# Optimization experiments

Hardware: AMD Instinct MI355X
Metric: run time of the kernel (lower is better)

The kernel has to match this reference:

```python
import jax, jax.numpy as jnp
import numpy as np

B, C, H, W = 2, 192, 96, 96
HEADS, DG, KH, KW = 12, 12, 3, 3
K = KH * KW
PAD, DIL = KH // 2, 1
MLP_HIDDEN = 2 * C  # mlp_ratio = 2


def setup_inputs() -> dict:
    key = jax.random.key(0)
    ks = jax.random.split(key, 14)
    s = 0.02
    return {
        "q": jax.random.normal(ks[0], (B, C, H, W), jnp.float32),
        "k": jax.random.normal(ks[1], (B, C, H, W), jnp.float32),
        "v": jax.random.normal(ks[2], (B, C, H, W), jnp.float32),
        "offset": jax.random.normal(ks[3], (B, DG * 2 * K, H, W), jnp.float32),
        "Wq": jax.random.normal(ks[4], (C, C), jnp.float32) * s,
        "bq": jax.random.normal(ks[5], (C,), jnp.float32) * s,
        "Wk": jax.random.normal(ks[6], (C, C), jnp.float32) * s,
        "bk": jax.random.normal(ks[7], (C,), jnp.float32) * s,
        "Wv": jax.random.normal(ks[8], (C, C), jnp.float32) * s,
        "bv": jax.random.normal(ks[9], (C,), jnp.float32) * s,
        "W1": jax.random.normal(ks[10], (C, MLP_HIDDEN), jnp.float32) * s,
        "b1": jax.random.normal(ks[11], (MLP_HIDDEN,), jnp.float32) * s,
        "W2": jax.random.normal(ks[12], (MLP_HIDDEN, C), jnp.float32) * s,
        "b2": jax.random.normal(ks[13], (C,), jnp.float32) * s,
    }


def _bilinear_sample(img, py, px):
    """img: [B,G,Cg,H,W]; py,px: [B,G,K,H,W] fractional sample coords.
    Returns [B,G,Cg,K,H,W]; zero outside image (DCN-style per-corner masking)."""
    b, g, cg, h, w = img.shape
    y0 = jnp.floor(py)
    x0 = jnp.floor(px)
    wy1 = py - y0
    wx1 = px - x0
    wy0 = 1.0 - wy1
    wx0 = 1.0 - wx1
    imgf = img.reshape(b, g, cg, h * w)

    def corner(yi, xi, wgt):
        valid = ((yi >= 0) & (yi <= h - 1) & (xi >= 0) & (xi <= w - 1)).astype(img.dtype)
        yc = jnp.clip(yi, 0, h - 1).astype(jnp.int32)
        xc = jnp.clip(xi, 0, w - 1).astype(jnp.int32)
        idx = (yc * w + xc).reshape(b, g, 1, -1)  # [B,G,1,K*H*W]
        gth = jnp.take_along_axis(imgf, idx, axis=3)  # [B,G,Cg,K*H*W]
        return gth * (valid * wgt).reshape(b, g, 1, -1)

    out = (corner(y0, x0, wy0 * wx0)
           + corner(y0, x0 + 1, wy0 * wx1)
           + corner(y0 + 1, x0, wy1 * wx0)
           + corner(y0 + 1, x0 + 1, wy1 * wx1))
    return out.reshape(b, g, cg, py.shape[2], h, w)


def _forward(q, k, v, offset, Wq, bq, Wk, bk, Wv, bv, W1, b1, W2, b2):
    def lin(x, Wm, bb):  # per-pixel Linear over channel dim
        return jnp.einsum('bchw,cd->bdhw', x, Wm) + bb[None, :, None, None]

    qp = lin(q, Wq, bq)
    kp = lin(k, Wk, bk)
    vp = lin(v, Wv, bv)

    # DCN-v1 offset layout: [B, G, K, 2(y,x), H, W]
    off = offset.reshape(B, DG, K, 2, H, W)
    ii, jj = jnp.meshgrid(jnp.arange(KH), jnp.arange(KW), indexing='ij')
    ii = ii.reshape(K)
    jj = jj.reshape(K)
    base_y = (jnp.arange(H)[None, :] - PAD + (ii * DIL)[:, None]).astype(jnp.float32)  # [K,H]
    base_x = (jnp.arange(W)[None, :] - PAD + (jj * DIL)[:, None]).astype(jnp.float32)  # [K,W]
    py = base_y[None, None, :, :, None] + off[:, :, :, 0]  # [B,G,K,H,W]
    px = base_x[None, None, :, None, :] + off[:, :, :, 1]

    cg = C // DG
    k_s = _bilinear_sample(kp.reshape(B, DG, cg, H, W), py, px)  # [B,G,cg,K,H,W]
    v_s = _bilinear_sample(vp.reshape(B, DG, cg, H, W), py, px)

    hd = C // HEADS
    k_s = k_s.reshape(B, HEADS, hd, K, H, W)
    v_s = v_s.reshape(B, HEADS, hd, K, H, W)
    qh = qp.reshape(B, HEADS, hd, H, W)

    scale = hd ** -0.5
    scores = jnp.einsum('bndhw,bndkhw->bnkhw', qh, k_s) * scale
    attn = jax.nn.softmax(scores, axis=2)  # over K sampled points (clip_size=1)
    out = jnp.einsum('bnkhw,bndkhw->bndhw', attn, v_s).reshape(B, C, H, W)

    # residual MLP (GELU exact, as torch nn.GELU default)
    xf = out.transpose(0, 2, 3, 1)  # [B,H,W,C]
    h1 = jax.nn.gelu(xf @ W1 + b1, approximate=False)
    mlp = (h1 @ W2 + b2).transpose(0, 3, 1, 2)
    return out + mlp


def reference(q, k, v, offset, Wq, bq, Wk, bk, Wv, bv, W1, b1, W2, b2):
    return _forward(q, k, v, offset, Wq, bq, Wk, bk, Wv, bv, W1, b1, W2, b2)
```

## Files before the change

kernel.cpp:

```cpp
#include <hip/hip_runtime.h>
#include <hip/hip_bf16.h>
#include <math.h>

#define B_    2
#define C_    192
#define H_    96
#define W_    96
#define HW_   (H_ * W_)
#define NPIX_ (B_ * HW_)
#define G_    12
#define CG_   16
#define KPTS_ 9
#define MLPH_ 384

typedef __attribute__((ext_vector_type(8))) short s16x8;
typedef __attribute__((ext_vector_type(4))) float f32x4;

__device__ __forceinline__ ushort f2b(float f) {
    __hip_bfloat16 h = __float2bfloat16(f);
    return *reinterpret_cast<ushort*>(&h);
}
__device__ __forceinline__ float b2f(ushort u) {
    return __uint_as_float(((uint)u) << 16);
}
__device__ __forceinline__ float b2f_lo(uint u) { return __uint_as_float(u << 16); }
__device__ __forceinline__ float b2f_hi(uint u) { return __uint_as_float(u & 0xffff0000u); }

#define GLOAD16(gp, lp)                                                          \
    __builtin_amdgcn_global_load_lds(                                            \
        (const __attribute__((address_space(1))) void*)(gp),                     \
        (__attribute__((address_space(3))) void*)(lp), 16, 0, 0)

__global__ __launch_bounds__(256) void pack_kernel(
    const float* __restrict__ q, const float* __restrict__ k,
    const float* __restrict__ v, ushort* __restrict__ Xcl)
{
    __shared__ ushort sm[64][196];
    const int t   = threadIdx.x;
    const int hw0 = blockIdx.x * 64;
    const int b   = blockIdx.y;
    const int z   = blockIdx.z;
    const float* X = (z == 0) ? q : (z == 1) ? k : v;

    const int hwl = t & 63;
    #pragma unroll 4
    for (int j = 0; j < 48; ++j) {
        const int c = (t >> 6) + j * 4;
        sm[hwl][c] = f2b(X[(b * C_ + c) * HW_ + hw0 + hwl]);
    }
    __syncthreads();
    #pragma unroll
    for (int jj = 0; jj < 12; ++jj) {
        const int idx = t + 256 * jj;
        const int row = idx / 48, cq = idx - row * 48;
        const int pix = b * HW_ + hw0 + row;
        *(uint2*)&Xcl[((z * NPIX_) + pix) * C_ + cq * 4] = *(uint2*)&sm[row][cq * 4];
    }
}

__global__ __launch_bounds__(256) void wpack_kernel(
    const float* __restrict__ Wq, const float* __restrict__ Wk,
    const float* __restrict__ Wv, const float* __restrict__ W1,
    const float* __restrict__ W2, ushort* __restrict__ Wt)
{
    const int i = blockIdx.x * 256 + threadIdx.x;
    if (i < 110592) {
        const int s = i / 36864, j = i - s * 36864;
        const float* src = (s == 0) ? Wq : (s == 1) ? Wk : Wv;
        const int d = j / 192, c = j - d * 192;
        Wt[i] = f2b(src[c * 192 + d]);
    } else if (i < 184320) {
        const int j = i - 110592, d = j / 192, c = j - d * 192;
        Wt[i] = f2b(W1[c * 384 + d]);
    } else if (i < 258048) {
        const int j = i - 184320, d = j / 384, c = j - d * 384;
        Wt[i] = f2b(W2[c * 192 + d]);
    }
}

template<int KK>
__device__ __forceinline__ void stage_tiles64(const ushort* Az, const ushort* Bz,
                                              ushort* dst, int t, int m0, int n0, int kt)
{
    #pragma unroll
    for (int j = 0; j < 4; ++j) {
        const int q = t + 256 * j;
        const int r = q >> 3, p = q & 7;
        const int s = p ^ (r & 7);
        GLOAD16(Az + (size_t)(m0 + r) * KK + kt * 64 + s * 8, dst + q * 8);
    }
    #pragma unroll
    for (int j = 0; j < 2; ++j) {
        const int q = t + 256 * j;
        const int r = q >> 3, p = q & 7;
        const int s = p ^ (r & 7);
        GLOAD16(Bz + (size_t)(n0 + r) * KK + kt * 64 + s * 8, dst + 8192 + q * 8);
    }
}

template<int KK, int EPI>
__global__ __launch_bounds__(256) void gemm_kernel(
    const ushort* __restrict__ A,  const ushort* __restrict__ BT,
    const float* __restrict__ bias0, const float* __restrict__ bias1,
    const float* __restrict__ bias2,
    ushort* __restrict__ Ob,
    const ushort* __restrict__ res, float* __restrict__ Onchw,
    int zAstr, int zBstr, int zOstr)
{
    __shared__ char lds_raw[49152];
    ushort* smem = (ushort*)lds_raw;

    const int t  = threadIdx.x;
    const int l  = t & 63;
    const int wid = t >> 6;
    const int wm = wid >> 1, wn = wid & 1;
    const int m0 = blockIdx.x * 128;
    const int n0 = blockIdx.y * 64;
    const int z  = blockIdx.z;
    const int Ntot = gridDim.y * 64;
    constexpr int NKT = KK / 64;

    const ushort* Az = A  + (size_t)z * zAstr;
    const ushort* Bz = BT + (size_t)z * zBstr;
    const float* bias = (z == 0) ? bias0 : (z == 1) ? bias1 : bias2;

    int aoff[4][2], boff[2][2];
    #pragma unroll
    for (int f = 0; f < 4; ++f) {
        const int r = wm * 64 + f * 16 + (l & 15);
        #pragma unroll
        for (int ks = 0; ks < 2; ++ks) {
            const int c = ks * 4 + (l >> 4);
            aoff[f][ks] = r * 64 + (c ^ (r & 7)) * 8;
        }
    }
    #pragma unroll
    for (int g = 0; g < 2; ++g) {
        const int r = wn * 32 + g * 16 + (l & 15);
        #pragma unroll
        for (int ks = 0; ks < 2; ++ks) {
            const int c = ks * 4 + (l >> 4);
            boff[g][ks] = 8192 + r * 64 + (c ^ (r & 7)) * 8;
        }
    }

    f32x4 acc[4][2] = {};

    stage_tiles64<KK>(Az, Bz, smem, t, m0, n0, 0);
    __syncthreads();

    for (int kt = 0; kt < NKT; ++kt) {
        if (kt + 1 < NKT)
            stage_tiles64<KK>(Az, Bz, smem + ((kt + 1) & 1) * 12288, t, m0, n0, kt + 1);

        const ushort* buf = smem + (kt & 1) * 12288;
        s16x8 af[4][2], bf[2][2];
        #pragma unroll
        for (int f = 0; f < 4; ++f)
            #pragma unroll
            for (int ks = 0; ks < 2; ++ks) af[f][ks] = *(const s16x8*)(buf + aoff[f][ks]);
        #pragma unroll
        for (int g = 0; g < 2; ++g)
            #pragma unroll
            for (int ks = 0; ks < 2; ++ks) bf[g][ks] = *(const s16x8*)(buf + boff[g][ks]);
        #pragma unroll
        for (int ks = 0; ks < 2; ++ks)
            #pragma unroll
            for (int f = 0; f < 4; ++f)
                #pragma unroll
                for (int g = 0; g < 2; ++g)
                    acc[f][g] = __builtin_amdgcn_mfma_f32_16x16x32_bf16(af[f][ks], bf[g][ks], acc[f][g], 0, 0, 0);
        __syncthreads();
    }

    const int rowg = l >> 4, ncol = l & 15;
    float bv[2];
    #pragma unroll
    for (int g = 0; g < 2; ++g) bv[g] = bias[n0 + wn * 32 + g * 16 + ncol];

    if (EPI == 0) {
        ushort* O = Ob + (size_t)z * zOstr;
        #pragma unroll
        for (int f = 0; f < 4; ++f)
            #pragma unroll
            for (int g = 0; g < 2; ++g)
                #pragma unroll
                for (int r = 0; r < 4; ++r) {
                    const int m = m0 + wm * 64 + f * 16 + rowg * 4 + r;
                    const int n = n0 + wn * 32 + g * 16 + ncol;
                    O[(size_t)m * Ntot + n] = f2b(acc[f][g][r] + bv[g]);
                }
    } else if (EPI == 1) {
        #pragma unroll
        for (int f = 0; f < 4; ++f)
            #pragma unroll
            for (int g = 0; g < 2; ++g)
                #pragma unroll
                for (int r = 0; r < 4; ++r) {
                    const int m = m0 + wm * 64 + f * 16 + rowg * 4 + r;
                    const int n = n0 + wn * 32 + g * 16 + ncol;
                    const float x = acc[f][g][r] + bv[g];
                    Ob[(size_t)m * Ntot + n] = f2b(0.5f * x * (1.f + erff(x * 0.70710678118f)));
                }
    } else {
        float* tsp = (float*)lds_raw;
        #pragma unroll
        for (int f = 0; f < 4; ++f)
            #pragma unroll
            for (int g = 0; g < 2; ++g)
                #pragma unroll
                for (int r = 0; r < 4; ++r) {
                    const int ml = wm * 64 + f * 16 + rowg * 4 + r;
                    const int nl = wn * 32 + g * 16 + ncol;
                    const float rv = b2f(res[(size_t)(m0 + ml) * C_ + n0 + nl]);
                    tsp[nl * 132 + ml] = acc[f][g][r] + bv[g] + rv;
                }
        __syncthreads();
        const int b   = m0 / HW_;
        const int hw0 = m0 - b * HW_;
        #pragma unroll
        for (int jj = 0; jj < 8; ++jj) {
            const int i4 = t + 256 * jj;
            const int nn = i4 >> 5, mc = i4 & 31;
            float4 val = *(float4*)&tsp[nn * 132 + mc * 4];
            *(float4*)&Onchw[(size_t)b * C_ * HW_ + (size_t)(n0 + nn) * HW_ + hw0 + mc * 4] = val;
        }
    }
}

__global__ __launch_bounds__(256, 2) void deform_attn_kernel(
    const ushort* __restrict__ qp, const ushort* __restrict__ kp,
    const ushort* __restrict__ vp, const float* __restrict__ offset,
    ushort* __restrict__ aob)
{
    const int t   = threadIdx.x;
    const int bid = blockIdx.x;
    const int xb  = (bid & 7) * 432 + (bid >> 3);
    const int pair = xb * 64 + (t >> 2);
    const int lane4 = t & 3;
    const int g   = pair % G_;
    const int pix = pair / G_;
    const int b   = pix / HW_;
    const int hw  = pix - b * HW_;
    const int h   = hw / W_;
    const int w   = hw - h * W_;
    const int gc0 = g * CG_ + lane4 * 4;

    float q0, q1, q2, q3;
    {
        uint2 qu = *(const uint2*)(qp + pix * C_ + gc0);
        q0 = b2f_lo(qu.x); q1 = b2f_hi(qu.x);
        q2 = b2f_lo(qu.y); q3 = b2f_hi(qu.y);
    }

    float offy[3] = {0.f, 0.f, 0.f}, offx[3] = {0.f, 0.f, 0.f};
    {
        const int obase = (b * (G_ * 2 * KPTS_) + g * (2 * KPTS_)) * HW_ + hw;
        #pragma unroll
        for (int s = 0; s < 3; ++s) {
            const int kk = lane4 + s * 4;
            if (kk < KPTS_) {
                offy[s] = offset[obase + (kk * 2) * HW_];
                offx[s] = offset[obase + (kk * 2 + 1) * HW_];
            }
        }
    }

    int   addr[KPTS_][4];
    float wgt[KPTS_][4];
    #pragma unroll
    for (int kk = 0; kk < KPTS_; ++kk) {
        const float oy = __shfl(offy[kk >> 2], kk & 3, 4);
        const float ox = __shfl(offx[kk >> 2], kk & 3, 4);
        const float py = (float)(h - 1 + kk / 3) + oy;
        const float px = (float)(w - 1 + kk % 3) + ox;
        const float fy = floorf(py), fx = floorf(px);
        const int   y0 = (int)fy,   x0 = (int)fx;
        const float wy1 = py - fy, wx1 = px - fx;
        const float wy0 = 1.f - wy1, wx0 = 1.f - wx1;

        const float wy0m = ((unsigned)y0       < (unsigned)H_) ? wy0 : 0.f;
        const float wy1m = ((unsigned)(y0 + 1) < (unsigned)H_) ? wy1 : 0.f;
        const float wx0m = ((unsigned)x0       < (unsigned)W_) ? wx0 : 0.f;
        const float wx1m = ((unsigned)(x0 + 1) < (unsigned)W_) ? wx1 : 0.f;
        const int yc0 = min(max(y0, 0), H_ - 1);
        const int yc1 = min(max(y0 + 1, 0), H_ - 1);
        const int xc0 = min(max(x0, 0), W_ - 1);
        const int xc1 = min(max(x0 + 1, 0), W_ - 1);

        addr[kk][0] = (yc0 * W_ + xc0) * C_ + gc0;  wgt[kk][0] = wy0m * wx0m;
        addr[kk][1] = (yc0 * W_ + xc1) * C_ + gc0;  wgt[kk][1] = wy0m * wx1m;
        addr[kk][2] = (yc1 * W_ + xc0) * C_ + gc0;  wgt[kk][2] = wy1m * wx0m;
        addr[kk][3] = (yc1 * W_ + xc1) * C_ + gc0;  wgt[kk][3] = wy1m * wx1m;
    }

    const ushort* kp_b = kp + (size_t)b * HW_ * C_;
    const ushort* vp_b = vp + (size_t)b * HW_ * C_;

    float score[KPTS_];
    #pragma unroll
    for (int kk = 0; kk < KPTS_; ++kk) {
        float s = 0.f;
        #pragma unroll
        for (int c = 0; c < 4; ++c) {
            const uint2 ku = *(const uint2*)(kp_b + addr[kk][c]);
            float d = q0 * b2f_lo(ku.x);
            d = fmaf(q1, b2f_hi(ku.x), d);
            d = fmaf(q2, b2f_lo(ku.y), d);
            d = fmaf(q3, b2f_hi(ku.y), d);
            s = fmaf(wgt[kk][c], d, s);
        }
        score[kk] = s;
    }
    #pragma unroll
    for (int kk = 0; kk < KPTS_; ++kk) {
        float sc = score[kk];
        sc += __shfl_xor(sc, 1, 4);
        sc += __shfl_xor(sc, 2, 4);
        score[kk] = sc * 0.25f;
    }

    float m = score[0];
    #pragma unroll
    for (int kk = 1; kk < KPTS_; ++kk) m = fmaxf(m, score[kk]);
    float ssum = 0.f;
    #pragma unroll
    for (int kk = 0; kk < KPTS_; ++kk) { score[kk] = __expf(score[kk] - m); ssum += score[kk]; }
    const float inv = 1.f / ssum;

    f32x4 o = {0.f, 0.f, 0.f, 0.f};
    #pragma unroll
    for (int kk = 0; kk < KPTS_; ++kk) {
        const float p = score[kk] * inv;
        #pragma unroll
        for (int c = 0; c < 4; ++c) {
            const float pw = p * wgt[kk][c];
            const uint2 vu = *(const uint2*)(vp_b + addr[kk][c]);
            o[0] = fmaf(pw, b2f_lo(vu.x), o[0]);
            o[1] = fmaf(pw, b2f_hi(vu.x), o[1]);
            o[2] = fmaf(pw, b2f_lo(vu.y), o[2]);
            o[3] = fmaf(pw, b2f_hi(vu.y), o[3]);
        }
    }

    uint2 ob;
    ob.x = (uint)f2b(o[0]) | ((uint)f2b(o[1]) << 16);
    ob.y = (uint)f2b(o[2]) | ((uint)f2b(o[3]) << 16);
    *(uint2*)(aob + pix * C_ + gc0) = ob;
}

extern "C" void kernel_launch(void* const* d_in, const int* in_sizes, int n_in,
                              void* d_out, int out_size, void* d_ws, size_t ws_size,
                              hipStream_t stream)
{
    const float* q      = (const float*)d_in[0];
    const float* k      = (const float*)d_in[1];
    const float* v      = (const float*)d_in[2];
    const float* offset = (const float*)d_in[3];
    const float* Wq     = (const float*)d_in[4];
    const float* bq     = (const float*)d_in[5];
    const float* Wk     = (const float*)d_in[6];
    const float* bk     = (const float*)d_in[7];
    const float* Wv     = (const float*)d_in[8];
    const float* bv     = (const float*)d_in[9];
    const float* W1     = (const float*)d_in[10];
    const float* b1     = (const float*)d_in[11];
    const float* W2     = (const float*)d_in[12];
    const float* b2     = (const float*)d_in[13];

    ushort* Xcl = (ushort*)d_ws;
    ushort* aob = Xcl;
    ushort* qkv = Xcl + 3 * NPIX_ * C_;
    ushort* Hb  = qkv + 3 * NPIX_ * C_;
    ushort* Wt  = Hb + (size_t)NPIX_ * MLPH_;
    ushort* W1T = Wt + 110592;
    ushort* W2T = Wt + 184320;

    pack_kernel<<<dim3(HW_ / 64, B_, 3), 256, 0, stream>>>(q, k, v, Xcl);
    wpack_kernel<<<1008, 256, 0, stream>>>(Wq, Wk, Wv, W1, W2, Wt);

    gemm_kernel<192, 0><<<dim3(NPIX_ / 128, 3, 3), 256, 0, stream>>>(
        Xcl, Wt, bq, bk, bv, qkv, nullptr, nullptr,
        NPIX_ * C_, C_ * C_, NPIX_ * C_);

    deform_attn_kernel<<<NPIX_ * G_ / 64, 256, 0, stream>>>(
        qkv, qkv + NPIX_ * C_, qkv + 2 * NPIX_ * C_, offset, aob);

    gemm_kernel<192, 1><<<dim3(NPIX_ / 128, 6, 1), 256, 0, stream>>>(
        aob, W1T, b1, b1, b1, Hb, nullptr, nullptr, 0, 0, 0);

    gemm_kernel<384, 2><<<dim3(NPIX_ / 128, 3, 1), 256, 0, stream>>>(
        Hb, W2T, b2, b2, b2, nullptr, aob, (float*)d_out, 0, 0, 0);
}
```

Baseline: 200.7 us.

## Interleave K/V per group, pre-transpose offsets, fuse prep kernels, use bf16 dot2

The QKV GEMM epilogue now writes K and V interleaved per 16-channel group, so each bilinear corner fetch reads K and V from adjacent addresses in one region. The offset tensor is transposed to pixel-major inside a merged prep kernel, which also absorbs the input and weight packing, so the attention kernel reads offsets with vector loads instead of strided scalar loads. The q·k dot product uses the bf16 dot2 intrinsic when available, and V values are loaded early alongside K. In exchange the prep kernel writes an extra offset buffer, and holding all 36 V corner values in registers raises register pressure in a kernel bounded to two blocks per SM.

```diff
diff --git a/kernel.cpp b/kernel.cpp
--- a/kernel.cpp
+++ b/kernel.cpp
@@ -12,6 +12,7 @@
 #define CG_   16
 #define KPTS_ 9
 #define MLPH_ 384
+#define OFFCH (G_ * 2 * KPTS_)
 
 typedef __attribute__((ext_vector_type(8))) short s16x8;
 typedef __attribute__((ext_vector_type(4))) float f32x4;
@@ -25,56 +26,81 @@
 }
 __device__ __forceinline__ float b2f_lo(uint u) { return __uint_as_float(u << 16); }
 __device__ __forceinline__ float b2f_hi(uint u) { return __uint_as_float(u & 0xffff0000u); }
+
+#if __has_builtin(__builtin_amdgcn_fdot2_f32_bf16)
+typedef __attribute__((ext_vector_type(2))) __bf16 bf16x2;
+#define HAVE_DOT2BF 1
+__device__ __forceinline__ float dot2bf(uint a, uint b, float c) {
+    return __builtin_amdgcn_fdot2_f32_bf16(__builtin_bit_cast(bf16x2, a),
+                                           __builtin_bit_cast(bf16x2, b), c, false);
+}
+#else
+#define HAVE_DOT2BF 0
+#endif
 
 #define GLOAD16(gp, lp)                                                          \
     __builtin_amdgcn_global_load_lds(                                            \
         (const __attribute__((address_space(1))) void*)(gp),                     \
         (__attribute__((address_space(3))) void*)(lp), 16, 0, 0)
 
-__global__ __launch_bounds__(256) void pack_kernel(
+__global__ __launch_bounds__(256) void prep_kernel(
     const float* __restrict__ q, const float* __restrict__ k,
-    const float* __restrict__ v, ushort* __restrict__ Xcl)
+    const float* __restrict__ v, const float* __restrict__ offset,
+    const float* __restrict__ Wq, const float* __restrict__ Wk,
+    const float* __restrict__ Wv, const float* __restrict__ W1,
+    const float* __restrict__ W2,
+    ushort* __restrict__ Xcl, float* __restrict__ offT, ushort* __restrict__ Wt)
 {
     __shared__ ushort sm[64][196];
-    const int t   = threadIdx.x;
-    const int hw0 = blockIdx.x * 64;
-    const int b   = blockIdx.y;
-    const int z   = blockIdx.z;
-    const float* X = (z == 0) ? q : (z == 1) ? k : v;
-
-    const int hwl = t & 63;
-    #pragma unroll 4
-    for (int j = 0; j < 48; ++j) {
-        const int c = (t >> 6) + j * 4;
-        sm[hwl][c] = f2b(X[(b * C_ + c) * HW_ + hw0 + hwl]);
-    }
-    __syncthreads();
-    #pragma unroll
-    for (int jj = 0; jj < 12; ++jj) {
-        const int idx = t + 256 * jj;
-        const int row = idx / 48, cq = idx - row * 48;
-        const int pix = b * HW_ + hw0 + row;
-        *(uint2*)&Xcl[((z * NPIX_) + pix) * C_ + cq * 4] = *(uint2*)&sm[row][cq * 4];
-    }
-}
-
-__global__ __launch_bounds__(256) void wpack_kernel(
-    const float* __restrict__ Wq, const float* __restrict__ Wk,
-    const float* __restrict__ Wv, const float* __restrict__ W1,
-    const float* __restrict__ W2, ushort* __restrict__ Wt)
-{
-    const int i = blockIdx.x * 256 + threadIdx.x;
-    if (i < 110592) {
-        const int s = i / 36864, j = i - s * 36864;
-        const float* src = (s == 0) ? Wq : (s == 1) ? Wk : Wv;
-        const int d = j / 192, c = j - d * 192;
-        Wt[i] = f2b(src[c * 192 + d]);
-    } else if (i < 184320) {
-        const int j = i - 110592, d = j / 192, c = j - d * 192;
-        Wt[i] = f2b(W1[c * 384 + d]);
-    } else if (i < 258048) {
-        const int j = i - 184320, d = j / 384, c = j - d * 384;
-        Wt[i] = f2b(W2[c * 192 + d]);
+    const int bx = blockIdx.x;
+    const int t  = threadIdx.x;
+
+    if (bx < 864) {
+        const int z   = bx / 288;
+        const int rem = bx - z * 288;
+        const int b   = rem / 144;
+        const int hw0 = (rem - b * 144) * 64;
+        const float* X = (z == 0) ? q : (z == 1) ? k : v;
+
+        const int hwl = t & 63;
+        #pragma unroll 4
+        for (int j = 0; j < 48; ++j) {
+            const int c = (t >> 6) + j * 4;
+            sm[hwl][c] = f2b(X[(b * C_ + c) * HW_ + hw0 + hwl]);
+        }
+        __syncthreads();
+        #pragma unroll
+        for (int jj = 0; jj < 12; ++jj) {
+            const int idx = t + 256 * jj;
+            const int row = idx / 48, cq = idx - row * 48;
+            const int pix = b * HW_ + hw0 + row;
+            *(uint2*)&Xcl[((z * NPIX_) + pix) * C_ + cq * 4] = *(uint2*)&sm[row][cq * 4];
+        }
+    } else if (bx < 1152) {
+        const int rem = bx - 864;
+        const int b   = rem / 144;
+        const int hw0 = (rem - b * 144) * 64;
+        #pragma unroll
+        for (int j = 0; j < 54; ++j) {
+            const int i = t + 256 * j;
+            const int pixl = i / OFFCH, p = i - pixl * OFFCH;
+            offT[(size_t)(b * HW_ + hw0 + pixl) * OFFCH + p] =
+                offset[(size_t)(b * OFFCH + p) * HW_ + hw0 + pixl];
+        }
+    } else {
+        const int i = (bx - 1152) * 256 + t;
+        if (i < 110592) {
+            const int s = i / 36864, j = i - s * 36864;
+            const float* src = (s == 0) ? Wq : (s == 1) ? Wk : Wv;
+            const int d = j / 192, c = j - d * 192;
+            Wt[i] = f2b(src[c * 192 + d]);
+        } else if (i < 184320) {
+            const int j = i - 110592, d = j / 192, c = j - d * 192;
+            Wt[i] = f2b(W1[c * 384 + d]);
+        } else if (i < 258048) {
+            const int j = i - 184320, d = j / 384, c = j - d * 384;
+            Wt[i] = f2b(W2[c * 192 + d]);
+        }
     }
 }
 
@@ -84,17 +110,17 @@
 {
     #pragma unroll
     for (int j = 0; j < 4; ++j) {
-        const int q = t + 256 * j;
-        const int r = q >> 3, p = q & 7;
+        const int qq = t + 256 * j;
+        const int r = qq >> 3, p = qq & 7;
         const int s = p ^ (r & 7);
-        GLOAD16(Az + (size_t)(m0 + r) * KK + kt * 64 + s * 8, dst + q * 8);
+        GLOAD16(Az + (size_t)(m0 + r) * KK + kt * 64 + s * 8, dst + qq * 8);
     }
     #pragma unroll
     for (int j = 0; j < 2; ++j) {
-        const int q = t + 256 * j;
-        const int r = q >> 3, p = q & 7;
+        const int qq = t + 256 * j;
+        const int r = qq >> 3, p = qq & 7;
         const int s = p ^ (r & 7);
-        GLOAD16(Bz + (size_t)(n0 + r) * KK + kt * 64 + s * 8, dst + 8192 + q * 8);
+        GLOAD16(Bz + (size_t)(n0 + r) * KK + kt * 64 + s * 8, dst + 8192 + qq * 8);
     }
 }
 
@@ -103,9 +129,9 @@
     const ushort* __restrict__ A,  const ushort* __restrict__ BT,
     const float* __restrict__ bias0, const float* __restrict__ bias1,
     const float* __restrict__ bias2,
-    ushort* __restrict__ Ob,
+    ushort* __restrict__ Ob, ushort* __restrict__ Okv,
     const ushort* __restrict__ res, float* __restrict__ Onchw,
-    int zAstr, int zBstr, int zOstr)
+    int zAstr, int zBstr)
 {
     __shared__ char lds_raw[49152];
     ushort* smem = (ushort*)lds_raw;
@@ -178,19 +204,34 @@
     #pragma unroll
     for (int g = 0; g < 2; ++g) bv[g] = bias[n0 + wn * 32 + g * 16 + ncol];
 
-    if (EPI == 0) {
-        ushort* O = Ob + (size_t)z * zOstr;
-        #pragma unroll
-        for (int f = 0; f < 4; ++f)
-            #pragma unroll
-            for (int g = 0; g < 2; ++g)
+    if constexpr (EPI == 0) {
+        if (z == 0) {
+            #pragma unroll
+            for (int f = 0; f < 4; ++f)
                 #pragma unroll
-                for (int r = 0; r < 4; ++r) {
-                    const int m = m0 + wm * 64 + f * 16 + rowg * 4 + r;
-                    const int n = n0 + wn * 32 + g * 16 + ncol;
-                    O[(size_t)m * Ntot + n] = f2b(acc[f][g][r] + bv[g]);
+                for (int g = 0; g < 2; ++g)
+                    #pragma unroll
+                    for (int r = 0; r < 4; ++r) {
+                        const int m = m0 + wm * 64 + f * 16 + rowg * 4 + r;
+                        const int n = n0 + wn * 32 + g * 16 + ncol;
+                        Ob[(size_t)m * C_ + n] = f2b(acc[f][g][r] + bv[g]);
+                    }
+        } else {
+            const int voff = (z == 2) ? 16 : 0;
+            #pragma unroll
+            for (int f = 0; f < 4; ++f)
+                #pragma unroll
+                for (int g = 0; g < 2; ++g) {
+                    const int grp = (n0 >> 4) + wn * 2 + g;
+                    #pragma unroll
+                    for (int r = 0; r < 4; ++r) {
+                        const int m = m0 + wm * 64 + f * 16 + rowg * 4 + r;
+                        Okv[(size_t)m * (2 * C_) + grp * 32 + voff + ncol] =
+                            f2b(acc[f][g][r] + bv[g]);
+                    }
                 }
-    } else if (EPI == 1) {
+        }
+    } else if constexpr (EPI == 1) {
         #pragma unroll
         for (int f = 0; f < 4; ++f)
             #pragma unroll
@@ -229,9 +270,8 @@
 }
 
 __global__ __launch_bounds__(256, 2) void deform_attn_kernel(
-    const ushort* __restrict__ qp, const ushort* __restrict__ kp,
-    const ushort* __restrict__ vp, const float* __restrict__ offset,
-    ushort* __restrict__ aob)
+    const ushort* __restrict__ qb, const ushort* __restrict__ kvb,
+    const float* __restrict__ offT, ushort* __restrict__ aob)
 {
     const int t   = threadIdx.x;
     const int bid = blockIdx.x;
@@ -246,23 +286,18 @@
     const int w   = hw - h * W_;
     const int gc0 = g * CG_ + lane4 * 4;
 
-    float q0, q1, q2, q3;
-    {
-        uint2 qu = *(const uint2*)(qp + pix * C_ + gc0);
-        q0 = b2f_lo(qu.x); q1 = b2f_hi(qu.x);
-        q2 = b2f_lo(qu.y); q3 = b2f_hi(qu.y);
-    }
-
+    uint2 qu = *(const uint2*)(qb + (size_t)pix * C_ + gc0);
+
+    const float* ob_ = offT + (size_t)pix * OFFCH + g * (2 * KPTS_);
     float offy[3] = {0.f, 0.f, 0.f}, offx[3] = {0.f, 0.f, 0.f};
     {
-        const int obase = (b * (G_ * 2 * KPTS_) + g * (2 * KPTS_)) * HW_ + hw;
-        #pragma unroll
-        for (int s = 0; s < 3; ++s) {
-            const int kk = lane4 + s * 4;
-            if (kk < KPTS_) {
-                offy[s] = offset[obase + (kk * 2) * HW_];
-                offx[s] = offset[obase + (kk * 2 + 1) * HW_];
-            }
+        float2 p0 = *(const float2*)(ob_ + lane4 * 2);
+        float2 p1 = *(const float2*)(ob_ + (lane4 + 4) * 2);
+        offy[0] = p0.x; offx[0] = p0.y;
+        offy[1] = p1.x; offx[1] = p1.y;
+        if (lane4 == 0) {
+            float2 p2 = *(const float2*)(ob_ + 16);
+            offy[2] = p2.x; offx[2] = p2.y;
         }
     }
 
@@ -288,26 +323,30 @@
         const int xc0 = min(max(x0, 0), W_ - 1);
         const int xc1 = min(max(x0 + 1, 0), W_ - 1);
 
-        addr[kk][0] = (yc0 * W_ + xc0) * C_ + gc0;  wgt[kk][0] = wy0m * wx0m;
-        addr[kk][1] = (yc0 * W_ + xc1) * C_ + gc0;  wgt[kk][1] = wy0m * wx1m;
-        addr[kk][2] = (yc1 * W_ + xc0) * C_ + gc0;  wgt[kk][2] = wy1m * wx0m;
-        addr[kk][3] = (yc1 * W_ + xc1) * C_ + gc0;  wgt[kk][3] = wy1m * wx1m;
-    }
-
-    const ushort* kp_b = kp + (size_t)b * HW_ * C_;
-    const ushort* vp_b = vp + (size_t)b * HW_ * C_;
+        const int kvbase = g * 32 + lane4 * 4;
+        addr[kk][0] = ((b * HW_ + yc0 * W_ + xc0) * (2 * C_)) + kvbase;  wgt[kk][0] = wy0m * wx0m;
+        addr[kk][1] = ((b * HW_ + yc0 * W_ + xc1) * (2 * C_)) + kvbase;  wgt[kk][1] = wy0m * wx1m;
+        addr[kk][2] = ((b * HW_ + yc1 * W_ + xc0) * (2 * C_)) + kvbase;  wgt[kk][2] = wy1m * wx0m;
+        addr[kk][3] = ((b * HW_ + yc1 * W_ + xc1) * (2 * C_)) + kvbase;  wgt[kk][3] = wy1m * wx1m;
+    }
 
     float score[KPTS_];
+    uint2 vu[KPTS_][4];
     #pragma unroll
     for (int kk = 0; kk < KPTS_; ++kk) {
         float s = 0.f;
         #pragma unroll
         for (int c = 0; c < 4; ++c) {
-            const uint2 ku = *(const uint2*)(kp_b + addr[kk][c]);
-            float d = q0 * b2f_lo(ku.x);
-            d = fmaf(q1, b2f_hi(ku.x), d);
-            d = fmaf(q2, b2f_lo(ku.y), d);
-            d = fmaf(q3, b2f_hi(ku.y), d);
+            const uint2 ku = *(const uint2*)(kvb + addr[kk][c]);
+            vu[kk][c]      = *(const uint2*)(kvb + addr[kk][c] + 16);
+#if HAVE_DOT2BF
+            const float d = dot2bf(ku.y, qu.y, dot2bf(ku.x, qu.x, 0.f));
+#else
+            float d = b2f_lo(qu.x) * b2f_lo(ku.x);
+            d = fmaf(b2f_hi(qu.x), b2f_hi(ku.x), d);
+            d = fmaf(b2f_lo(qu.y), b2f_lo(ku.y), d);
+            d = fmaf(b2f_hi(qu.y), b2f_hi(ku.y), d);
+#endif
             s = fmaf(wgt[kk][c], d, s);
         }
         score[kk] = s;
@@ -335,18 +374,17 @@
         #pragma unroll
         for (int c = 0; c < 4; ++c) {
             const float pw = p * wgt[kk][c];
-            const uint2 vu = *(const uint2*)(vp_b + addr[kk][c]);
-            o[0] = fmaf(pw, b2f_lo(vu.x), o[0]);
-            o[1] = fmaf(pw, b2f_hi(vu.x), o[1]);
-            o[2] = fmaf(pw, b2f_lo(vu.y), o[2]);
-            o[3] = fmaf(pw, b2f_hi(vu.y), o[3]);
-        }
-    }
-
-    uint2 ob;
-    ob.x = (uint)f2b(o[0]) | ((uint)f2b(o[1]) << 16);
-    ob.y = (uint)f2b(o[2]) | ((uint)f2b(o[3]) << 16);
-    *(uint2*)(aob + pix * C_ + gc0) = ob;
+            o[0] = fmaf(pw, b2f_lo(vu[kk][c].x), o[0]);
+            o[1] = fmaf(pw, b2f_hi(vu[kk][c].x), o[1]);
+            o[2] = fmaf(pw, b2f_lo(vu[kk][c].y), o[2]);
+            o[3] = fmaf(pw, b2f_hi(vu[kk][c].y), o[3]);
+        }
+    }
+
+    uint2 obv;
+    obv.x = (uint)f2b(o[0]) | ((uint)f2b(o[1]) << 16);
+    obv.y = (uint)f2b(o[2]) | ((uint)f2b(o[3]) << 16);
+    *(uint2*)(aob + (size_t)pix * C_ + gc0) = obv;
 }
 
 extern "C" void kernel_launch(void* const* d_in, const int* in_sizes, int n_in,
@@ -368,27 +406,29 @@
     const float* W2     = (const float*)d_in[12];
     const float* b2     = (const float*)d_in[13];
 
-    ushort* Xcl = (ushort*)d_ws;
+    ushort* ws0 = (ushort*)d_ws;
+    ushort* Xcl = ws0;
     ushort* aob = Xcl;
-    ushort* qkv = Xcl + 3 * NPIX_ * C_;
-    ushort* Hb  = qkv + 3 * NPIX_ * C_;
-    ushort* Wt  = Hb + (size_t)NPIX_ * MLPH_;
+    ushort* qb  = Xcl + (size_t)3 * NPIX_ * C_;
+    ushort* kvb = qb  + (size_t)NPIX_ * C_;
+    ushort* Hb  = kvb + (size_t)NPIX_ * 2 * C_;
+    ushort* Wt  = Hb  + (size_t)NPIX_ * MLPH_;
     ushort* W1T = Wt + 110592;
     ushort* W2T = Wt + 184320;
-
-    pack_kernel<<<dim3(HW_ / 64, B_, 3), 256, 0, stream>>>(q, k, v, Xcl);
-    wpack_kernel<<<1008, 256, 0, stream>>>(Wq, Wk, Wv, W1, W2, Wt);
+    float*  offT = (float*)(Wt + 258048);
+
+    prep_kernel<<<2160, 256, 0, stream>>>(q, k, v, offset, Wq, Wk, Wv, W1, W2,
+                                          Xcl, offT, Wt);
 
     gemm_kernel<192, 0><<<dim3(NPIX_ / 128, 3, 3), 256, 0, stream>>>(
-        Xcl, Wt, bq, bk, bv, qkv, nullptr, nullptr,
-        NPIX_ * C_, C_ * C_, NPIX_ * C_);
-
-    deform_attn_kernel<<<NPIX_ * G_ / 64, 256, 0, stream>>>(
-        qkv, qkv + NPIX_ * C_, qkv + 2 * NPIX_ * C_, offset, aob);
+        Xcl, Wt, bq, bk, bv, qb, kvb, nullptr, nullptr,
+        NPIX_ * C_, C_ * C_);
+
+    deform_attn_kernel<<<NPIX_ * G_ / 64, 256, 0, stream>>>(qb, kvb, offT, aob);
 
     gemm_kernel<192, 1><<<dim3(NPIX_ / 128, 6, 1), 256, 0, stream>>>(
-        aob, W1T, b1, b1, b1, Hb, nullptr, nullptr, 0, 0, 0);
+        aob, W1T, b1, b1, b1, Hb, nullptr, nullptr, nullptr, 0, 0);
 
     gemm_kernel<384, 2><<<dim3(NPIX_ / 128, 3, 1), 256, 0, stream>>>(
-        Hb, W2T, b2, b2, b2, nullptr, aob, (float*)d_out, 0, 0, 0);
-}
+        Hb, W2T, b2, b2, b2, nullptr, nullptr, aob, (float*)d_out, 0, 0);
+}
```

Measured after the change: 208.0 us. 3.7% more time.
